# Performance work log

Hardware: AMD Instinct MI355X
Metric: run time of the kernel (lower is better)

The kernel has to match this reference:

```python
import jax, jax.numpy as jnp
import numpy as np

H = 4            # num_attention_heads
EPS_LN = 1e-6    # LayerNorm eps
EPS_IN = 1e-5    # InstanceNorm2d eps (no affine)


def layer_norm(x, g, b):
    m = x.mean(-1, keepdims=True)
    v = ((x - m) ** 2).mean(-1, keepdims=True)
    return (x - m) * jax.lax.rsqrt(v + EPS_LN) * g + b


def instance_norm(s):
    # s: [B,H,C,KV]; InstanceNorm2d(H): normalize per (b,h) over spatial dims (C,KV)
    m = s.mean(axis=(2, 3), keepdims=True)
    v = s.var(axis=(2, 3), keepdims=True)
    return (s - m) * jax.lax.rsqrt(v + EPS_IN)


def _forward(emb1, emb2, emb3, emb4,
             an1_g, an1_b, Wq1, Wo1, fn1_g, fn1_b, fc11_w, fc11_b, fc12_w, fc12_b,
             an2_g, an2_b, Wq2, Wo2, fn2_g, fn2_b, fc21_w, fc21_b, fc22_w, fc22_b,
             an3_g, an3_b, Wq3, Wo3, fn3_g, fn3_b, fc31_w, fc31_b, fc32_w, fc32_b,
             an4_g, an4_b, Wq4, Wo4, fn4_g, fn4_b, fc41_w, fc41_b, fc42_w, fc42_b,
             anA_g, anA_b, Wk, Wv):
    embs = [emb1, emb2, emb3, emb4]
    branches = [
        (an1_g, an1_b, Wq1, Wo1, fn1_g, fn1_b, fc11_w, fc11_b, fc12_w, fc12_b),
        (an2_g, an2_b, Wq2, Wo2, fn2_g, fn2_b, fc21_w, fc21_b, fc22_w, fc22_b),
        (an3_g, an3_b, Wq3, Wo3, fn3_g, fn3_b, fc31_w, fc31_b, fc32_w, fc32_b),
        (an4_g, an4_b, Wq4, Wo4, fn4_g, fn4_b, fc41_w, fc41_b, fc42_w, fc42_b),
    ]
    emb_all = jnp.concatenate(embs, axis=-1)          # [B, n, KV]
    KV = emb_all.shape[-1]
    ea = layer_norm(emb_all, anA_g, anA_b)
    # per-head K/V projections (torch Linear: y = x @ W^T), stacked over heads
    K = jnp.einsum('bnk,hjk->bhnj', ea, Wk)           # [B,H,n,KV]
    V = jnp.einsum('bnk,hjk->bhnj', ea, Wv)           # [B,H,n,KV]
    scale = 1.0 / np.sqrt(KV).astype(np.float32)
    outs = []
    for e, (ag, ab, Wq, Wo, fg, fb, w1, b1, w2, b2) in zip(embs, branches):
        cx = layer_norm(e, ag, ab)                    # [B,n,C]
        Q = jnp.einsum('bnc,hdc->bhnd', cx, Wq)       # [B,H,n,C]
        # channel-attention scores: Q^T K over tokens -> [B,H,C,KV]
        scores = jnp.einsum('bhnd,bhnj->bhdj', Q, K) * scale
        probs = jax.nn.softmax(instance_norm(scores), axis=-1)
        # context [B,H,C,n] averaged over heads -> [B,n,C] (fused into einsum)
        ctx = jnp.einsum('bhdj,bhnj->bnd', probs, V) / H
        O = ctx @ Wo.T                                # out projection
        x = e + O                                     # residual
        h = layer_norm(x, fg, fb)
        h = jax.nn.gelu(h @ w1.T + b1, approximate=False)
        h = h @ w2.T + b2
        outs.append(x + h)                            # FFN residual
    return outs


def setup_inputs() -> dict:
    key = jax.random.key(0)
    B, N = 4, 784
    Cs = [64, 128, 256, 512]
    KV = sum(Cs)
    ks = iter(jax.random.split(key, 64))
    def nrm(shape, scale=0.02):
        return jax.random.normal(next(ks), shape, dtype=jnp.float32) * scale
    inp = {}
    for i, C in enumerate(Cs, 1):
        inp[f'emb{i}'] = jax.random.normal(next(ks), (B, N, C), dtype=jnp.float32)
        inp[f'an{i}_g'] = jnp.ones((C,), jnp.float32)
        inp[f'an{i}_b'] = jnp.zeros((C,), jnp.float32)
        inp[f'Wq{i}'] = nrm((H, C, C))
        inp[f'Wo{i}'] = nrm((C, C))
        inp[f'fn{i}_g'] = jnp.ones((C,), jnp.float32)
        inp[f'fn{i}_b'] = jnp.zeros((C,), jnp.float32)
        inp[f'fc{i}1_w'] = nrm((4 * C, C))
        inp[f'fc{i}1_b'] = nrm((4 * C,), 1e-6)
        inp[f'fc{i}2_w'] = nrm((C, 4 * C))
        inp[f'fc{i}2_b'] = nrm((C,), 1e-6)
    inp['anA_g'] = jnp.ones((KV,), jnp.float32)
    inp['anA_b'] = jnp.zeros((KV,), jnp.float32)
    inp['Wk'] = nrm((H, KV, KV))
    inp['Wv'] = nrm((H, KV, KV))
    return inp


def reference(emb1, emb2, emb3, emb4,
              an1_g, an1_b, Wq1, Wo1, fn1_g, fn1_b, fc11_w, fc11_b, fc12_w, fc12_b,
              an2_g, an2_b, Wq2, Wo2, fn2_g, fn2_b, fc21_w, fc21_b, fc22_w, fc22_b,
              an3_g, an3_b, Wq3, Wo3, fn3_g, fn3_b, fc31_w, fc31_b, fc32_w, fc32_b,
              an4_g, an4_b, Wq4, Wo4, fn4_g, fn4_b, fc41_w, fc41_b, fc42_w, fc42_b,
              anA_g, anA_b, Wk, Wv):
    outs = _forward(emb1, emb2, emb3, emb4,
                    an1_g, an1_b, Wq1, Wo1, fn1_g, fn1_b, fc11_w, fc11_b, fc12_w, fc12_b,
                    an2_g, an2_b, Wq2, Wo2, fn2_g, fn2_b, fc21_w, fc21_b, fc22_w, fc22_b,
                    an3_g, an3_b, Wq3, Wo3, fn3_g, fn3_b, fc31_w, fc31_b, fc32_w, fc32_b,
                    an4_g, an4_b, Wq4, Wo4, fn4_g, fn4_b, fc41_w, fc41_b, fc42_w, fc42_b,
                    anA_g, anA_b, Wk, Wv)
    return tuple(outs)
```

## Files before the change

### kernel.cpp

```cpp
#include <hip/hip_runtime.h>
#include <hip/hip_bf16.h>


using bf16 = __hip_bfloat16;
typedef __attribute__((ext_vector_type(8))) short short8;
typedef __attribute__((ext_vector_type(4))) float f32x4;

__device__ inline float bf2f(unsigned short u) {
    return __uint_as_float(((unsigned int)u) << 16);
}
__device__ inline unsigned short f2b(float f) {
    unsigned int u = __float_as_uint(f);
    return (unsigned short)((u + 0x7fffu + ((u >> 16) & 1u)) >> 16);
}
__device__ inline float ld1f(const float* p) { return *p; }
__device__ inline float ld1f(const bf16* p) { return bf2f(*(const unsigned short*)p); }
__device__ inline void st1(float* p, float v) { *p = v; }
__device__ inline void st1(bf16* p, float v) { *((unsigned short*)p) = f2b(v); }
__device__ inline float4 ld4f(const bf16* p) {
    ushort4 u = *(const ushort4*)p;
    return make_float4(bf2f(u.x), bf2f(u.y), bf2f(u.z), bf2f(u.w));
}

__device__ __forceinline__ void cp16(const void* g, void* l) {
    __builtin_amdgcn_global_load_lds(
        (const __attribute__((address_space(1))) void*)g,
        (__attribute__((address_space(3))) void*)l, 16, 0, 0);
}

__device__ inline float blockSum256(float v, float* red) {
    #pragma unroll
    for (int o = 32; o > 0; o >>= 1) v += __shfl_down(v, o);
    int t = threadIdx.x;
    if ((t & 63) == 0) red[t >> 6] = v;
    __syncthreads();
    float r = red[0] + red[1] + red[2] + red[3];
    __syncthreads();
    return r;
}
__device__ inline float blockMax256(float v, float* red) {
    #pragma unroll
    for (int o = 32; o > 0; o >>= 1) v = fmaxf(v, __shfl_down(v, o));
    int t = threadIdx.x;
    if ((t & 63) == 0) red[t >> 6] = v;
    __syncthreads();
    float r = fmaxf(fmaxf(red[0], red[1]), fmaxf(red[2], red[3]));
    __syncthreads();
    return r;
}

struct CvtN {
    const float* s[18];
    unsigned short* d[18];
    long n[18];
    float* z;
};
__global__ __launch_bounds__(256)
void cvtn_kernel(CvtN a) {
    if (a.z && blockIdx.x == 0 && threadIdx.x < 128) a.z[threadIdx.x] = 0.f;
    long tid = (long)blockIdx.x * 256 + threadIdx.x;
    long stride = (long)gridDim.x * 256;
    for (int g = 0; g < 18; g++) {
        const float* s = a.s[g];
        unsigned short* d = a.d[g];
        long n = a.n[g];
        for (long i = tid * 4; i < n; i += stride * 4) {
            float4 v = *(const float4*)(s + i);
            *(ushort4*)(d + i) = make_ushort4(f2b(v.x), f2b(v.y), f2b(v.z), f2b(v.w));
        }
    }
}

template <class CT, class RT, bool TO>
__global__ __launch_bounds__(256, 3)
void mfma4(const bf16* __restrict__ A, long Ah, long Ab, int lda,
           const bf16* __restrict__ B, long Bh, long Bb, int ldb,
           CT* __restrict__ Cp, long Ch, long Cb, int ldc,
           const float* __restrict__ bias, const RT* __restrict__ res,
           int M, int N, int K, int Mpad, int Npad, int qx, int hy,
           float alpha, int dogelu, float* __restrict__ stat) {
    __shared__ short Asl[3][128][32];
    __shared__ short Bsl[3][128][32];
    int gx = gridDim.x, gy = gridDim.y;
    int orig = ((int)blockIdx.z * gy + (int)blockIdx.y) * gx + (int)blockIdx.x;
    int bx, by, bz;
    if (qx) {
        int c = orig & 7, r2 = orig >> 3;
        bx = (c & 3) * qx + r2 % qx;
        by = (c >> 2) * hy + r2 / qx;
        bz = 0;
    } else {
        int nxy = gx * gy, nwg = nxy * (int)gridDim.z;
        int q = nwg >> 3, r8 = nwg & 7;
        int xcd = orig & 7, pos = orig >> 3;
        int wgid = (xcd < r8 ? xcd * (q + 1) : r8 * (q + 1) + (xcd - r8) * q) + pos;
        bz = wgid / nxy;
        int rem = wgid - bz * nxy;
        by = rem / gx; bx = rem - by * gx;
    }
    int z = bz;
    A += (long)(z & 3) * Ah + (long)(z >> 2) * Ab;
    B += (long)(z & 3) * Bh + (long)(z >> 2) * Bb;
    Cp += (long)(z & 3) * Ch + (long)(z >> 2) * Cb;
    int m0 = by * 128, n0 = bx * 128;
    int t = threadIdx.x, lane = t & 63, wv = t >> 6;
    int col = lane & 15, quad = lane >> 4;
    int wm = wv >> 1, wn = wv & 1;
    f32x4 acc[4][4];
    #pragma unroll
    for (int i = 0; i < 4; i++)
        #pragma unroll
        for (int j = 0; j < 4; j++) acc[i][j] = (f32x4){0.f, 0.f, 0.f, 0.f};

    const bool fA = (m0 + 128 <= Mpad);
    const bool fB = (n0 + 128 <= Npad);
    int srow = lane >> 2;
    int scol = ((lane & 3) ^ ((lane >> 3) & 3)) << 3;
    int rslot = (quad ^ ((col >> 1) & 3)) << 3;

    auto stageA = [&](int s3, int kt) {
        int k0 = kt * 32;
        if (fA && k0 + 32 <= K) {
            #pragma unroll
            for (int r = 0; r < 2; r++) {
                int R0 = (r * 4 + wv) * 16;
                cp16(A + (long)(m0 + R0 + srow) * lda + k0 + scol, &Asl[s3][R0][0]);
            }
        } else {
            #pragma unroll
            for (int r = 0; r < 2; r++) {
                int idx = r * 256 + t;
                int row = idx >> 2, sl = idx & 3;
                int f2 = (row >> 1) & 3;
                short8 v = {};
                if (m0 + row < M && k0 + sl * 8 < K)
                    v = *(const short8*)(A + (long)(m0 + row) * lda + k0 + sl * 8);
                *(short8*)&Asl[s3][row][(sl ^ f2) * 8] = v;
            }
            asm volatile("s_waitcnt lgkmcnt(0)" ::: "memory");
        }
    };
    auto stageB = [&](int s3, int kt) {
        int k0 = kt * 32;
        if (fB && k0 + 32 <= K) {
            #pragma unroll
            for (int r = 0; r < 2; r++) {
                int R0 = (r * 4 + wv) * 16;
                cp16(B + (long)(n0 + R0 + srow) * ldb + k0 + scol, &Bsl[s3][R0][0]);
            }
        } else {
            #pragma unroll
            for (int r = 0; r < 2; r++) {
                int idx = r * 256 + t;
                int row = idx >> 2, sl = idx & 3;
                int f2 = (row >> 1) & 3;
                short8 v = {};
                if (n0 + row < N && k0 + sl * 8 < K)
                    v = *(const short8*)(B + (long)(n0 + row) * ldb + k0 + sl * 8);
                *(short8*)&Bsl[s3][row][(sl ^ f2) * 8] = v;
            }
            asm volatile("s_waitcnt lgkmcnt(0)" ::: "memory");
        }
    };

    int nk = (K + 31) >> 5;
    stageA(0, 0); stageB(0, 0);
    stageA(1, 1); stageB(1, 1);
    __syncthreads();

    for (int kt = 0; kt < nk; kt++) {
        int cur = kt % 3;
        short8 af[4], bf4[4];
        #pragma unroll
        for (int mi = 0; mi < 4; mi++)
            af[mi] = *(const short8*)&Asl[cur][wm * 64 + mi * 16 + col][rslot];
        #pragma unroll
        for (int ni = 0; ni < 4; ni++)
            bf4[ni] = *(const short8*)&Bsl[cur][wn * 64 + ni * 16 + col][rslot];
        int pend = 0;
        if (kt + 2 < nk) {
            int s3 = (kt + 2) % 3;
            stageA(s3, kt + 2); stageB(s3, kt + 2);
            if ((kt + 2) * 32 + 32 <= K) pend = (fA ? 2 : 0) + (fB ? 2 : 0);
        }
        __builtin_amdgcn_s_barrier();
        asm volatile("s_waitcnt lgkmcnt(0)" ::: "memory");
        __builtin_amdgcn_sched_barrier(0);
        __builtin_amdgcn_s_setprio(1);
        #pragma unroll
        for (int mi = 0; mi < 4; mi++)
            #pragma unroll
            for (int ni = 0; ni < 4; ni++)
                acc[mi][ni] = __builtin_amdgcn_mfma_f32_16x16x32_bf16(
                    af[mi], bf4[ni], acc[mi][ni], 0, 0, 0);
        __builtin_amdgcn_s_setprio(0);
        if (kt + 1 < nk) {
            if (pend == 4)      asm volatile("s_waitcnt vmcnt(4)" ::: "memory");
            else if (pend == 2) asm volatile("s_waitcnt vmcnt(2)" ::: "memory");
            else                asm volatile("s_waitcnt vmcnt(0)" ::: "memory");
            __builtin_amdgcn_s_barrier();
        }
    }
    float psum = 0.f, psq = 0.f;
    #pragma unroll
    for (int mi = 0; mi < 4; mi++) {
        int gmB = m0 + wm * 64 + mi * 16 + quad * 4;
        #pragma unroll
        for (int ni = 0; ni < 4; ni++) {
            int gn = n0 + wn * 64 + ni * 16 + col;
            if constexpr (TO) {
                if (gmB < M && gn < N) {
                    ushort4 w = make_ushort4(f2b(acc[mi][ni][0] * alpha),
                                             f2b(acc[mi][ni][1] * alpha),
                                             f2b(acc[mi][ni][2] * alpha),
                                             f2b(acc[mi][ni][3] * alpha));
                    *(ushort4*)((unsigned short*)Cp + (long)gn * ldc + gmB) = w;
                }
            } else {
                if (gn < N) {
                    float bz2 = bias ? bias[gn] : 0.f;
                    #pragma unroll
                    for (int r = 0; r < 4; r++) {
                        int gm = gmB + r;
                        if (gm < M) {
                            float v = acc[mi][ni][r] * alpha + bz2;
                            if (dogelu) v = 0.5f * v * (1.f + erff(v * 0.70710678118f));
                            if (res) v += ld1f(res + (long)gm * ldc + gn);
                            st1(Cp + (long)gm * ldc + gn, v);
                            psum += v; psq += v * v;
                        }
                    }
                }
            }
        }
    }
    if (stat) {
        __syncthreads();
        #pragma unroll
        for (int o = 32; o > 0; o >>= 1) {
            psum += __shfl_down(psum, o);
            psq  += __shfl_down(psq, o);
        }
        float* red = (float*)Asl;
        if ((t & 63) == 0) { red[wv] = psum; red[4 + wv] = psq; }
        __syncthreads();
        if (t == 0) {
            atomicAdd(&stat[2 * z],     red[0] + red[1] + red[2] + red[3]);
            atomicAdd(&stat[2 * z + 1], red[4] + red[5] + red[6] + red[7]);
        }
    }
}

struct G4 {
    const bf16* A[4]; const bf16* B[4]; void* Cv[4];
    const float* bias[4]; const void* res[4];
    int M[4], N[4], K[4], lda[4], ldb[4], ldc[4], nbx[4];
    int cum[5];
};
template <class CT, class RT>
__global__ __launch_bounds__(256, 3)
void mfma4g(G4 gp, int dogelu) {
    __shared__ short Asl[3][128][32];
    __shared__ short Bsl[3][128][32];
    int nwg = gridDim.x;
    int orig = blockIdx.x;
    int q = nwg >> 3, r8 = nwg & 7;
    int xcd = orig & 7, pos = orig >> 3;
    int wgid = (xcd < r8 ? xcd * (q + 1) : r8 * (q + 1) + (xcd - r8) * q) + pos;
    int gi = 0;
    if (wgid >= gp.cum[1]) gi = 1;
    if (wgid >= gp.cum[2]) gi = 2;
    if (wgid >= gp.cum[3]) gi = 3;
    int local = wgid - gp.cum[gi];
    int nbx = gp.nbx[gi];
    int by = local / nbx, bx = local - by * nbx;
    const bf16* A = gp.A[gi];
    const bf16* B = gp.B[gi];
    CT* Cp = (CT*)gp.Cv[gi];
    const float* bias = gp.bias[gi];
    const RT* res = (const RT*)gp.res[gi];
    int M = gp.M[gi], N = gp.N[gi], K = gp.K[gi];
    int lda = gp.lda[gi], ldb = gp.ldb[gi], ldc = gp.ldc[gi];
    int m0 = by * 128, n0 = bx * 128;
    int t = threadIdx.x, lane = t & 63, wv = t >> 6;
    int col = lane & 15, quad = lane >> 4;
    int wm = wv >> 1, wn = wv & 1;
    f32x4 acc[4][4];
    #pragma unroll
    for (int i = 0; i < 4; i++)
        #pragma unroll
        for (int j = 0; j < 4; j++) acc[i][j] = (f32x4){0.f, 0.f, 0.f, 0.f};

    int srow = lane >> 2;
    int scol = ((lane & 3) ^ ((lane >> 3) & 3)) << 3;
    int rslot = (quad ^ ((col >> 1) & 3)) << 3;

    auto stageA = [&](int s3, int kt) {
        int k0 = kt * 32;
        #pragma unroll
        for (int r = 0; r < 2; r++) {
            int R0 = (r * 4 + wv) * 16;
            cp16(A + (long)(m0 + R0 + srow) * lda + k0 + scol, &Asl[s3][R0][0]);
        }
    };
    auto stageB = [&](int s3, int kt) {
        int k0 = kt * 32;
        #pragma unroll
        for (int r = 0; r < 2; r++) {
            int R0 = (r * 4 + wv) * 16;
            cp16(B + (long)(n0 + R0 + srow) * ldb + k0 + scol, &Bsl[s3][R0][0]);
        }
    };

    int nk = K >> 5;
    stageA(0, 0); stageB(0, 0);
    stageA(1, 1); stageB(1, 1);
    __syncthreads();

    for (int kt = 0; kt < nk; kt++) {
        int cur = kt % 3;
        short8 af[4], bf4[4];
        #pragma unroll
        for (int mi = 0; mi < 4; mi++)
            af[mi] = *(const short8*)&Asl[cur][wm * 64 + mi * 16 + col][rslot];
        #pragma unroll
        for (int ni = 0; ni < 4; ni++)
            bf4[ni] = *(const short8*)&Bsl[cur][wn * 64 + ni * 16 + col][rslot];
        bool st = (kt + 2 < nk);
        if (st) {
            int s3 = (kt + 2) % 3;
            stageA(s3, kt + 2); stageB(s3, kt + 2);
        }
        __builtin_amdgcn_s_barrier();
        asm volatile("s_waitcnt lgkmcnt(0)" ::: "memory");
        __builtin_amdgcn_sched_barrier(0);
        __builtin_amdgcn_s_setprio(1);
        #pragma unroll
        for (int mi = 0; mi < 4; mi++)
            #pragma unroll
            for (int ni = 0; ni < 4; ni++)
                acc[mi][ni] = __builtin_amdgcn_mfma_f32_16x16x32_bf16(
                    af[mi], bf4[ni], acc[mi][ni], 0, 0, 0);
        __builtin_amdgcn_s_setprio(0);
        if (kt + 1 < nk) {
            if (st) asm volatile("s_waitcnt vmcnt(4)" ::: "memory");
            else    asm volatile("s_waitcnt vmcnt(0)" ::: "memory");
            __builtin_amdgcn_s_barrier();
        }
    }
    #pragma unroll
    for (int mi = 0; mi < 4; mi++) {
        int gmB = m0 + wm * 64 + mi * 16 + quad * 4;
        #pragma unroll
        for (int ni = 0; ni < 4; ni++) {
            int gn = n0 + wn * 64 + ni * 16 + col;
            if (gn < N) {
                float bz2 = bias ? bias[gn] : 0.f;
                #pragma unroll
                for (int r = 0; r < 4; r++) {
                    int gm = gmB + r;
                    if (gm < M) {
                        float v = acc[mi][ni][r] + bz2;
                        if (dogelu) v = 0.5f * v * (1.f + erff(v * 0.70710678118f));
                        if (res) v += ld1f(res + (long)gm * ldc + gn);
                        st1(Cp + (long)gm * ldc + gn, v);
                    }
                }
            }
        }
    }
}

template <int TM, int TN, class CT, class RT, bool TO>
__global__ __launch_bounds__(256)
void mfma2(const bf16* __restrict__ A, long Ah, long Ab, int lda,
           const bf16* __restrict__ B, long Bh, long Bb, int ldb,
           CT* __restrict__ Cp, long Ch, long Cb, int ldc,
           const float* __restrict__ bias, const RT* __restrict__ res,
           int M, int N, int K, float alpha, int dogelu,
           float* __restrict__ stat) {
    constexpr int MI = TM / 32, NI = TN / 32;
    __shared__ short As[2][TM * 32];
    __shared__ short Bs[2][TN * 32];
    int z = blockIdx.z;
    A += (long)(z & 3) * Ah + (long)(z >> 2) * Ab;
    B += (long)(z & 3) * Bh + (long)(z >> 2) * Bb;
    Cp += (long)(z & 3) * Ch + (long)(z >> 2) * Cb;
    int m0 = blockIdx.y * TM, n0 = blockIdx.x * TN;
    int t = threadIdx.x, lane = t & 63, wv = t >> 6;
    int col = lane & 15, quad = lane >> 4;
    int wm = wv >> 1, wn = wv & 1;
    f32x4 acc[MI][NI];
    #pragma unroll
    for (int i = 0; i < MI; i++)
        #pragma unroll
        for (int j = 0; j < NI; j++) acc[i][j] = (f32x4){0.f, 0.f, 0.f, 0.f};

    const bool fastblk = (m0 + TM <= M) && (n0 + TN <= N);
    int lrow = lane >> 2;
    int lcol = ((lane & 3) ^ ((lane >> 3) & 3)) << 3;
    int sr = t >> 2;
    int swz = ((t & 3) ^ ((t >> 3) & 3)) << 3;
    int sdst = (t & 3) << 3;
    int rdslot = (quad ^ ((col >> 1) & 3)) << 3;

    auto stage = [&](int b, int k0) {
        if (fastblk && (k0 + 32 <= K)) {
            #pragma unroll
            for (int u = 0; u < TM / 64; u++) {
                int c = wv + 4 * u;
                int r = c * 16 + lrow;
                cp16(A + (long)(m0 + r) * lda + k0 + lcol, &As[b][c * 512]);
            }
            #pragma unroll
            for (int u = 0; u < TN / 64; u++) {
                int c = wv + 4 * u;
                int r = c * 16 + lrow;
                cp16(B + (long)(n0 + r) * ldb + k0 + lcol, &Bs[b][c * 512]);
            }
        } else {
            #pragma unroll
            for (int u = 0; u < TM / 64; u++) {
                int r = sr + u * 64;
                float4 v = make_float4(0.f, 0.f, 0.f, 0.f);
                if (m0 + r < M && k0 + swz < K)
                    v = *(const float4*)(A + (long)(m0 + r) * lda + k0 + swz);
                *(float4*)&As[b][r * 32 + sdst] = v;
            }
            #pragma unroll
            for (int u = 0; u < TN / 64; u++) {
                int r = sr + u * 64;
                float4 v = make_float4(0.f, 0.f, 0.f, 0.f);
                if (n0 + r < N && k0 + swz < K)
                    v = *(const float4*)(B + (long)(n0 + r) * ldb + k0 + swz);
                *(float4*)&Bs[b][r * 32 + sdst] = v;
            }
        }
    };

    int nk = (K + 31) >> 5;
    stage(0, 0);
    __syncthreads();
    int cur = 0;
    for (int s = 0; s < nk; s++) {
        if (s + 1 < nk) stage(cur ^ 1, (s + 1) * 32);
        short8 af[MI], bfr[NI];
        #pragma unroll
        for (int mi = 0; mi < MI; mi++)
            af[mi] = *(const short8*)&As[cur][(wm * (TM / 2) + mi * 16 + col) * 32 + rdslot];
        #pragma unroll
        for (int ni = 0; ni < NI; ni++)
            bfr[ni] = *(const short8*)&Bs[cur][(wn * (TN / 2) + ni * 16 + col) * 32 + rdslot];
        #pragma unroll
        for (int mi = 0; mi < MI; mi++)
            #pragma unroll
            for (int ni = 0; ni < NI; ni++)
                acc[mi][ni] = __builtin_amdgcn_mfma_f32_16x16x32_bf16(
                    af[mi], bfr[ni], acc[mi][ni], 0, 0, 0);
        if (s + 1 < nk) __syncthreads();
        cur ^= 1;
    }
    float psum = 0.f, psq = 0.f;
    #pragma unroll
    for (int mi = 0; mi < MI; mi++) {
        int gmB = m0 + wm * (TM / 2) + mi * 16 + quad * 4;
        #pragma unroll
        for (int ni = 0; ni < NI; ni++) {
            int gn = n0 + wn * (TN / 2) + ni * 16 + col;
            if constexpr (TO) {
                if (gmB < M && gn < N) {
                    ushort4 w = make_ushort4(f2b(acc[mi][ni][0] * alpha),
                                             f2b(acc[mi][ni][1] * alpha),
                                             f2b(acc[mi][ni][2] * alpha),
                                             f2b(acc[mi][ni][3] * alpha));
                    *(ushort4*)((unsigned short*)Cp + (long)gn * ldc + gmB) = w;
                }
            } else {
                if (gn < N) {
                    float bz = bias ? bias[gn] : 0.f;
                    #pragma unroll
                    for (int r = 0; r < 4; r++) {
                        int gm = gmB + r;
                        if (gm < M) {
                            float v = acc[mi][ni][r] * alpha + bz;
                            if (dogelu) v = 0.5f * v * (1.f + erff(v * 0.70710678118f));
                            if (res) v += ld1f(res + (long)gm * ldc + gn);
                            st1(Cp + (long)gm * ldc + gn, v);
                            psum += v; psq += v * v;
                        }
                    }
                }
            }
        }
    }
    if (stat) {
        __syncthreads();
        #pragma unroll
        for (int o = 32; o > 0; o >>= 1) {
            psum += __shfl_down(psum, o);
            psq  += __shfl_down(psq, o);
        }
        float* red = (float*)As;
        if ((t & 63) == 0) { red[wv] = psum; red[4 + wv] = psq; }
        __syncthreads();
        if (t == 0) {
            atomicAdd(&stat[2 * z],     red[0] + red[1] + red[2] + red[3]);
            atomicAdd(&stat[2 * z + 1], red[4] + red[5] + red[6] + red[7]);
        }
    }
}

struct LNA {
    const float* e[4];
    const float* ag[4];
    const float* ab[4];
    const float* cg;
    const float* cbb;
    bf16* y[4];
    bf16* ea;
};
__global__ __launch_bounds__(256)
void ln_all_kernel(LNA a) {
    __shared__ float x[960];
    __shared__ float red[4];
    long row = blockIdx.x;
    int t = threadIdx.x;
    const int off[5] = {0, 64, 192, 448, 960};
    {
        const float* p1 = a.e[0] + row * 64;
        const float* p2 = a.e[1] + row * 128;
        const float* p3 = a.e[2] + row * 256;
        const float* p4 = a.e[3] + row * 512;
        if (t < 64) x[t] = p1[t];
        for (int i = t; i < 128; i += 256) x[64 + i]  = p2[i];
        for (int i = t; i < 256; i += 256) x[192 + i] = p3[i];
        for (int i = t; i < 512; i += 256) x[448 + i] = p4[i];
    }
    __syncthreads();
    float ssum[4], ssq[4];
    #pragma unroll
    for (int br = 0; br < 4; br++) {
        float s = 0.f, q = 0.f;
        for (int i = off[br] + t; i < off[br + 1]; i += 256) {
            float v = x[i]; s += v; q += v * v;
        }
        ssum[br] = blockSum256(s, red);
        ssq[br]  = blockSum256(q, red);
    }
    float S1 = ssum[0] + ssum[1] + ssum[2] + ssum[3];
    float S2 = ssq[0] + ssq[1] + ssq[2] + ssq[3];
    float muA = S1 * (1.f / 960.f);
    float rA = rsqrtf(S2 * (1.f / 960.f) - muA * muA + 1e-6f);
    for (int i = t; i < 960; i += 256)
        st1(a.ea + row * 960 + i, (x[i] - muA) * rA * a.cg[i] + a.cbb[i]);
    #pragma unroll
    for (int br = 0; br < 4; br++) {
        int C = off[br + 1] - off[br];
        float mu = ssum[br] / C;
        float rr = rsqrtf(ssq[br] / C - mu * mu + 1e-6f);
        const float* g = a.ag[br];
        const float* b = a.ab[br];
        bf16* y = a.y[br] + row * C;
        for (int i = t; i < C; i += 256)
            st1(y + i, (x[off[br] + i] - mu) * rr * g[i] + b[i]);
    }
}

struct LR4 {
    const bf16* X[4];
    const float* g[4];
    const float* b[4];
    bf16* Y[4];
    int C[4];
};
__global__ __launch_bounds__(256)
void ln_rows4_kernel(LR4 a) {
    __shared__ float x[512];
    __shared__ float red[4];
    int br = blockIdx.y;
    long row = blockIdx.x;
    int C = a.C[br];
    int t = threadIdx.x;
    const bf16* xr = a.X[br] + row * C;
    float s = 0.f, q = 0.f;
    for (int i = t; i < C; i += 256) { float v = ld1f(xr + i); x[i] = v; s += v; q += v * v; }
    float S1 = blockSum256(s, red), S2 = blockSum256(q, red);
    float mu = S1 / C;
    float r = rsqrtf(S2 / C - mu * mu + 1e-6f);
    const float* g = a.g[br];
    const float* b = a.b[br];
    bf16* y = a.Y[br] + row * C;
    for (int i = t; i < C; i += 256)
        st1(y + i, (x[i] - mu) * r * g[i] + b[i]);
}

__global__ __launch_bounds__(256)
void ctx_sum_kernel(const bf16* __restrict__ tmp, bf16* __restrict__ ctx, long NTC) {
    long i = ((long)blockIdx.x * 256 + threadIdx.x) * 4;
    float4 a = ld4f(tmp + i);
    float4 b = ld4f(tmp + NTC + i);
    float4 c = ld4f(tmp + 2 * NTC + i);
    float4 d = ld4f(tmp + 3 * NTC + i);
    ushort4 o = make_ushort4(f2b((a.x + b.x + c.x + d.x) * 0.25f),
                             f2b((a.y + b.y + c.y + d.y) * 0.25f),
                             f2b((a.z + b.z + c.z + d.z) * 0.25f),
                             f2b((a.w + b.w + c.w + d.w) * 0.25f));
    *(ushort4*)(ctx + i) = o;
}

__global__ __launch_bounds__(256)
void softmax_kernel(bf16* __restrict__ S, const float* __restrict__ stat, int C) {
    __shared__ float x[960];
    __shared__ float red[4];
    long r = blockIdx.x;
    int t = threadIdx.x;
    int z = (int)(r / C);
    int d = (int)(r % C);
    float n = 960.f * (float)C;
    float s0 = stat[2 * z], q0 = stat[2 * z + 1];
    float mu = s0 / n;
    float rs = rsqrtf(q0 / n - mu * mu + 1e-5f);
    int h = z & 3, b = z >> 2;
    bf16* row = S + (long)b * C * 3840 + (long)d * 3840 + h * 960;
    float mx = -3.4e38f;
    for (int i = t; i < 960; i += 256) {
        float v = ld1f(row + i) * rs; x[i] = v; mx = fmaxf(mx, v);
    }
    float M = blockMax256(mx, red);
    float s = 0.f;
    for (int i = t; i < 960; i += 256) { float e = __expf(x[i] - M); x[i] = e; s += e; }
    float Ssum = blockSum256(s, red);
    float inv = 1.f / Ssum;
    for (int i = t; i < 960; i += 256) st1(row + i, x[i] * inv);
}

extern "C" void kernel_launch(void* const* d_in, const int* in_sizes, int n_in,
                              void* d_out, int out_size, void* d_ws, size_t ws_size,
                              hipStream_t stream) {
    (void)in_sizes; (void)n_in; (void)out_size; (void)ws_size;
    const int Cs[4] = {64, 128, 256, 512};
    const float *emb[4], *ang[4], *anb[4], *Wq[4], *Wo[4], *fng[4], *fnb[4], *w1[4], *b1[4], *w2[4], *b2[4];
    for (int i = 0; i < 4; i++) {
        const int base = i * 11;
        emb[i] = (const float*)d_in[base + 0];
        ang[i] = (const float*)d_in[base + 1];
        anb[i] = (const float*)d_in[base + 2];
        Wq[i]  = (const float*)d_in[base + 3];
        Wo[i]  = (const float*)d_in[base + 4];
        fng[i] = (const float*)d_in[base + 5];
        fnb[i] = (const float*)d_in[base + 6];
        w1[i]  = (const float*)d_in[base + 7];
        b1[i]  = (const float*)d_in[base + 8];
        w2[i]  = (const float*)d_in[base + 9];
        b2[i]  = (const float*)d_in[base + 10];
    }
    const float* anAg = (const float*)d_in[44];
    const float* anAb = (const float*)d_in[45];
    const float* Wk   = (const float*)d_in[46];
    const float* Wv   = (const float*)d_in[47];

    const int NT = 3136;
    char* wsb = (char*)d_ws;
    unsigned short* wp = (unsigned short*)(wsb);
    float* statb = (float*)(wsb + 9052160);
    bf16*  KT    = (bf16*)(wsb + 9053184);
    bf16*  hid   = (bf16*)(wsb + 9053184);
    bf16*  Vb2   = (bf16*)(wsb + 33137664);
    bf16*  xball = (bf16*)(wsb + 33137664);
    bf16*  cx3   = (bf16*)(wsb + 39158784);
    bf16*  QT    = (bf16*)(wsb + 57222144);
    bf16*  wkb   = (bf16*)(wsb + 57222144);
    bf16*  Sb    = (bf16*)(wsb + 70067200);
    bf16*  ea    = (bf16*)(wsb + 70067200);
    bf16*  wvb   = (bf16*)(wsb + 76088320);
    bf16*  cxall = (bf16*)(wsb + 85795840);
    bf16*  cx2   = (bf16*)(wsb + 91816960);

    const long wb[4] = {0, 53248, 266240, 1118208};
    const long co[4] = {0, 64L * NT, 192L * NT, 448L * NT};
    const long ho[4] = {0, 802816, 2408448, 5619712};

    float* out = (float*)d_out;
    const long ooff[4] = {0, 200704, 602112, 1404928};
    const float scale = 0.03227486121f;

    {
        CvtN a;
        a.s[0] = Wk; a.d[0] = (unsigned short*)wkb; a.n[0] = 3686400;
        a.s[1] = Wv; a.d[1] = (unsigned short*)wvb; a.n[1] = 3686400;
        for (int i = 0; i < 4; i++) {
            const long C2 = (long)Cs[i] * Cs[i];
            a.s[2 + 4 * i] = Wq[i]; a.d[2 + 4 * i] = wp + wb[i];          a.n[2 + 4 * i] = 4 * C2;
            a.s[3 + 4 * i] = Wo[i]; a.d[3 + 4 * i] = wp + wb[i] + 4 * C2; a.n[3 + 4 * i] = C2;
            a.s[4 + 4 * i] = w1[i]; a.d[4 + 4 * i] = wp + wb[i] + 5 * C2; a.n[4 + 4 * i] = 4 * C2;
            a.s[5 + 4 * i] = w2[i]; a.d[5 + 4 * i] = wp + wb[i] + 9 * C2; a.n[5 + 4 * i] = 4 * C2;
        }
        a.z = statb;
        cvtn_kernel<<<1024, 256, 0, stream>>>(a);
    }
    {
        LNA a;
        for (int i = 0; i < 4; i++) {
            a.e[i] = emb[i]; a.ag[i] = ang[i]; a.ab[i] = anb[i];
            a.y[i] = cxall + co[i];
        }
        a.cg = anAg; a.cbb = anAb; a.ea = ea;
        ln_all_kernel<<<3136, 256, 0, stream>>>(a);
    }
    mfma4<bf16, float, true><<<dim3(32, 26, 1), 256, 0, stream>>>(
        ea, 0, 0, 960, wkb, 0, 0, 960, KT, 0, 0, NT,
        nullptr, (const float*)nullptr, NT, 3840, 960, 3328, 4096, 8, 13,
        1.f, 0, nullptr);
    mfma4<bf16, float, false><<<dim3(32, 26, 1), 256, 0, stream>>>(
        ea, 0, 0, 960, wvb, 0, 0, 960, Vb2, 0, 0, 3840,
        nullptr, (const float*)nullptr, NT, 3840, 960, 3328, 4096, 8, 13,
        1.f, 0, nullptr);

    for (int i = 0; i < 4; i++) {
        const int C = Cs[i];
        const long C2 = (long)C * C;
        bf16* wqb = (bf16*)(wp + wb[i]);
        float* st = statb + 32 * i;
        if (C >= 128) {
            mfma4<bf16, float, true><<<dim3(C / 128, 26, 4), 256, 0, stream>>>(
                cxall + co[i], 0, 0, C, wqb, C2, 0, C, QT, (long)C * NT, 0, NT,
                nullptr, (const float*)nullptr, NT, C, C, 3328, C, 0, 0,
                1.f, 0, nullptr);
            mfma4<bf16, float, false><<<dim3(8, C / 128, 16), 256, 0, stream>>>(
                QT, (long)C * NT, 784, NT, KT, 3010560, 784, NT,
                Sb, 960, (long)C * 3840, 3840,
                nullptr, (const float*)nullptr, C, 960, 784, C, 1024, 0, 0,
                scale, 0, st);
        } else {
            mfma2<64, 64, bf16, float, true><<<dim3(1, 49, 4), 256, 0, stream>>>(
                cxall + co[i], 0, 0, C, wqb, C2, 0, C, QT, (long)C * NT, 0, NT,
                nullptr, (const float*)nullptr, NT, C, C, 1.f, 0, nullptr);
            mfma2<64, 64, bf16, float, false><<<dim3(15, 1, 16), 256, 0, stream>>>(
                QT, (long)C * NT, 784, NT, KT, 3010560, 784, NT,
                Sb, 960, (long)C * 3840, 3840,
                nullptr, (const float*)nullptr, C, 960, 784, scale, 0, st);
        }
        softmax_kernel<<<16 * C, 256, 0, stream>>>(Sb, st, C);
        if (C >= 128)
            mfma4<bf16, float, false><<<dim3(C / 128, 7, 16), 256, 0, stream>>>(
                Vb2, 960, 784L * 3840, 3840, Sb, 960, (long)C * 3840, 3840,
                QT, (long)NT * C, 784L * C, C,
                nullptr, (const float*)nullptr, 784, C, 960, 896, C, 0, 0,
                1.f, 0, nullptr);
        else
            mfma2<64, 64, bf16, float, false><<<dim3(1, 13, 16), 256, 0, stream>>>(
                Vb2, 960, 784L * 3840, 3840, Sb, 960, (long)C * 3840, 3840,
                QT, (long)NT * C, 784L * C, C,
                nullptr, (const float*)nullptr, 784, C, 960, 1.f, 0, nullptr);
        ctx_sum_kernel<<<(int)(((long)NT * C) / 1024), 256, 0, stream>>>(
            QT, cx2 + co[i], (long)NT * C);
    }

    {
        G4 g;
        int cum = 0;
        for (int i = 0; i < 4; i++) {
            const int C = Cs[i];
            const long C2 = (long)C * C;
            g.A[i] = cx2 + co[i]; g.B[i] = (const bf16*)(wp + wb[i] + 4 * C2);
            g.Cv[i] = xball + co[i];
            g.bias[i] = nullptr; g.res[i] = emb[i];
            g.M[i] = NT; g.N[i] = C; g.K[i] = C;
            g.lda[i] = C; g.ldb[i] = C; g.ldc[i] = C;
            g.nbx[i] = (C >= 128) ? C / 128 : 1;
            g.cum[i] = cum; cum += g.nbx[i] * 26;
        }
        g.cum[4] = cum;
        mfma4g<bf16, float><<<cum, 256, 0, stream>>>(g, 0);
    }
    {
        LR4 a;
        for (int i = 0; i < 4; i++) {
            a.X[i] = xball + co[i]; a.g[i] = fng[i]; a.b[i] = fnb[i];
            a.Y[i] = cx3 + co[i]; a.C[i] = Cs[i];
        }
        ln_rows4_kernel<<<dim3(3136, 4), 256, 0, stream>>>(a);
    }
    {
        G4 g;
        int cum = 0;
        for (int i = 0; i < 4; i++) {
            const int C = Cs[i];
            const long C2 = (long)C * C;
            g.A[i] = cx3 + co[i]; g.B[i] = (const bf16*)(wp + wb[i] + 5 * C2);
            g.Cv[i] = hid + ho[i];
            g.bias[i] = b1[i]; g.res[i] = nullptr;
            g.M[i] = NT; g.N[i] = 4 * C; g.K[i] = C;
            g.lda[i] = C; g.ldb[i] = C; g.ldc[i] = 4 * C;
            g.nbx[i] = 4 * C / 128;
            g.cum[i] = cum; cum += g.nbx[i] * 26;
        }
        g.cum[4] = cum;
        mfma4g<bf16, float><<<cum, 256, 0, stream>>>(g, 1);
    }
    {
        G4 g;
        int cum = 0;
        for (int i = 0; i < 4; i++) {
            const int C = Cs[i];
            const long C2 = (long)C * C;
            g.A[i] = hid + ho[i]; g.B[i] = (const bf16*)(wp + wb[i] + 9 * C2);
            g.Cv[i] = out + ooff[i];
            g.bias[i] = b2[i]; g.res[i] = xball + co[i];
            g.M[i] = NT; g.N[i] = C; g.K[i] = 4 * C;
            g.lda[i] = 4 * C; g.ldb[i] = 4 * C; g.ldc[i] = C;
            g.nbx[i] = (C >= 128) ? C / 128 : 1;
            g.cum[i] = cum; cum += g.nbx[i] * 26;
        }
        g.cum[4] = cum;
        mfma4g<float, bf16><<<cum, 256, 0, stream>>>(g, 0);
    }
}
```

Measured before the change: 740.5 us.

## Fuse K and V projections into one 256x256-tile MFMA GEMM kernel

Replaces the two separate 128-tile GEMM launches for the K and V projections with a single 512-thread kernel. It uses 256x256 tiles and a double-buffered LDS pipeline that splits each 64-wide k-step into halves, with priority hints around the MFMA bursts. Wk and Wv are laid out contiguously so the combined N=7680 weight matrix can be treated as one GEMM. The epilogue routes columns below 3840 to the transposed K buffer and the rest to V. The goal is more data reuse per tile and one fewer launch, at the cost of higher register and LDS pressure and uncoalesced scalar V stores.

```diff
diff --git a/kernel.cpp b/kernel.cpp
--- a/kernel.cpp
+++ b/kernel.cpp
@@ -67,6 +67,154 @@
         for (long i = tid * 4; i < n; i += stride * 4) {
             float4 v = *(const float4*)(s + i);
             *(ushort4*)(d + i) = make_ushort4(f2b(v.x), f2b(v.y), f2b(v.z), f2b(v.w));
+        }
+    }
+}
+
+__global__ __launch_bounds__(512, 2)
+void mfma8kv(const bf16* __restrict__ A, const bf16* __restrict__ B,
+             bf16* __restrict__ KT, bf16* __restrict__ V) {
+    __shared__ short Asl[2][2][256][32];
+    __shared__ short Bsl[2][2][256][32];
+    const int M = 3136, N = 7680, lda = 960, ldb = 960;
+    int orig = (int)blockIdx.y * 32 + (int)blockIdx.x;
+    int c = orig & 7, r2 = orig >> 3;
+    int bx = (c & 3) * 8 + (r2 & 7);
+    int by = (c >> 2) * 7 + (r2 >> 3);
+    int m0 = by * 256, n0 = bx * 256;
+    if (m0 >= M || n0 >= N) return;
+    int t = threadIdx.x, lane = t & 63, wv = t >> 6;
+    int col = lane & 15, quad = lane >> 4;
+    int wm = wv >> 2, wn = wv & 3;
+    f32x4 acc[8][4];
+    #pragma unroll
+    for (int i = 0; i < 8; i++)
+        #pragma unroll
+        for (int j = 0; j < 4; j++) acc[i][j] = (f32x4){0.f, 0.f, 0.f, 0.f};
+
+    int srow = lane >> 2;
+    int scol = ((lane & 3) ^ ((lane >> 3) & 3)) << 3;
+    int rslot = (quad ^ ((col >> 1) & 3)) << 3;
+
+    auto stageA = [&](int s2, int kt, int kh) {
+        int k0 = kt * 64 + kh * 32;
+        #pragma unroll
+        for (int r = 0; r < 2; r++) {
+            int R0 = (r * 8 + wv) * 16;
+            cp16(A + (long)(m0 + R0 + srow) * lda + k0 + scol, &Asl[s2][kh][R0][0]);
+        }
+    };
+    auto stageB = [&](int s2, int kt, int kh) {
+        int k0 = kt * 64 + kh * 32;
+        #pragma unroll
+        for (int r = 0; r < 2; r++) {
+            int R0 = (r * 8 + wv) * 16;
+            cp16(B + (long)(n0 + R0 + srow) * ldb + k0 + scol, &Bsl[s2][kh][R0][0]);
+        }
+    };
+
+    const int nk = 15;
+    stageA(0, 0, 0); stageB(0, 0, 0); stageA(0, 0, 1); stageB(0, 0, 1);
+    __syncthreads();
+
+    for (int kt = 0; kt < nk; kt++) {
+        int cur = kt & 1, nxt = cur ^ 1;
+        bool st = (kt + 1 < nk);
+        short8 af[8], bf8[4];
+        #pragma unroll
+        for (int ni = 0; ni < 4; ni++)
+            bf8[ni] = *(const short8*)&Bsl[cur][0][wn * 64 + ni * 16 + col][rslot];
+        #pragma unroll
+        for (int mi = 0; mi < 4; mi++)
+            af[mi] = *(const short8*)&Asl[cur][0][wm * 128 + mi * 16 + col][rslot];
+        if (st) stageA(nxt, kt + 1, 0);
+        __builtin_amdgcn_s_barrier();
+        asm volatile("s_waitcnt lgkmcnt(0)" ::: "memory");
+        __builtin_amdgcn_sched_barrier(0);
+        __builtin_amdgcn_s_setprio(1);
+        #pragma unroll
+        for (int mi = 0; mi < 4; mi++)
+            #pragma unroll
+            for (int ni = 0; ni < 4; ni++)
+                acc[mi][ni] = __builtin_amdgcn_mfma_f32_16x16x32_bf16(
+                    af[mi], bf8[ni], acc[mi][ni], 0, 0, 0);
+        __builtin_amdgcn_s_setprio(0);
+        __builtin_amdgcn_s_barrier();
+        #pragma unroll
+        for (int mi = 4; mi < 8; mi++)
+            af[mi] = *(const short8*)&Asl[cur][0][wm * 128 + mi * 16 + col][rslot];
+        if (st) stageB(nxt, kt + 1, 0);
+        __builtin_amdgcn_s_barrier();
+        asm volatile("s_waitcnt lgkmcnt(0)" ::: "memory");
+        __builtin_amdgcn_sched_barrier(0);
+        __builtin_amdgcn_s_setprio(1);
+        #pragma unroll
+        for (int mi = 4; mi < 8; mi++)
+            #pragma unroll
+            for (int ni = 0; ni < 4; ni++)
+                acc[mi][ni] = __builtin_amdgcn_mfma_f32_16x16x32_bf16(
+                    af[mi], bf8[ni], acc[mi][ni], 0, 0, 0);
+        __builtin_amdgcn_s_setprio(0);
+        if (st) asm volatile("s_waitcnt vmcnt(4)" ::: "memory");
+        else    asm volatile("s_waitcnt vmcnt(0)" ::: "memory");
+        __builtin_amdgcn_s_barrier();
+        #pragma unroll
+        for (int ni = 0; ni < 4; ni++)
+            bf8[ni] = *(const short8*)&Bsl[cur][1][wn * 64 + ni * 16 + col][rslot];
+        #pragma unroll
+        for (int mi = 0; mi < 4; mi++)
+            af[mi] = *(const short8*)&Asl[cur][1][wm * 128 + mi * 16 + col][rslot];
+        if (st) stageA(nxt, kt + 1, 1);
+        __builtin_amdgcn_s_barrier();
+        asm volatile("s_waitcnt lgkmcnt(0)" ::: "memory");
+        __builtin_amdgcn_sched_barrier(0);
+        __builtin_amdgcn_s_setprio(1);
+        #pragma unroll
+        for (int mi = 0; mi < 4; mi++)
+            #pragma unroll
+            for (int ni = 0; ni < 4; ni++)
+                acc[mi][ni] = __builtin_amdgcn_mfma_f32_16x16x32_bf16(
+                    af[mi], bf8[ni], acc[mi][ni], 0, 0, 0);
+        __builtin_amdgcn_s_setprio(0);
+        __builtin_amdgcn_s_barrier();
+        #pragma unroll
+        for (int mi = 4; mi < 8; mi++)
+            af[mi] = *(const short8*)&Asl[cur][1][wm * 128 + mi * 16 + col][rslot];
+        if (st) stageB(nxt, kt + 1, 1);
+        __builtin_amdgcn_s_barrier();
+        asm volatile("s_waitcnt lgkmcnt(0)" ::: "memory");
+        __builtin_amdgcn_sched_barrier(0);
+        __builtin_amdgcn_s_setprio(1);
+        #pragma unroll
+        for (int mi = 4; mi < 8; mi++)
+            #pragma unroll
+            for (int ni = 0; ni < 4; ni++)
+                acc[mi][ni] = __builtin_amdgcn_mfma_f32_16x16x32_bf16(
+                    af[mi], bf8[ni], acc[mi][ni], 0, 0, 0);
+        __builtin_amdgcn_s_setprio(0);
+        if (st) asm volatile("s_waitcnt vmcnt(4)" ::: "memory");
+        __builtin_amdgcn_s_barrier();
+    }
+    #pragma unroll
+    for (int mi = 0; mi < 8; mi++) {
+        int gmB = m0 + wm * 128 + mi * 16 + quad * 4;
+        #pragma unroll
+        for (int ni = 0; ni < 4; ni++) {
+            int gn = n0 + wn * 64 + ni * 16 + col;
+            if (gn < 3840) {
+                if (gmB < M) {
+                    ushort4 w = make_ushort4(f2b(acc[mi][ni][0]), f2b(acc[mi][ni][1]),
+                                             f2b(acc[mi][ni][2]), f2b(acc[mi][ni][3]));
+                    *(ushort4*)((unsigned short*)KT + (long)gn * M + gmB) = w;
+                }
+            } else {
+                int vn = gn - 3840;
+                #pragma unroll
+                for (int r = 0; r < 4; r++) {
+                    int gm = gmB + r;
+                    if (gm < M) st1(V + (long)gm * 3840 + vn, acc[mi][ni][r]);
+                }
+            }
         }
     }
 }
@@ -669,10 +817,9 @@
     bf16*  xball = (bf16*)(wsb + 33137664);
     bf16*  cx3   = (bf16*)(wsb + 39158784);
     bf16*  QT    = (bf16*)(wsb + 57222144);
-    bf16*  wkb   = (bf16*)(wsb + 57222144);
+    bf16*  wkv   = (bf16*)(wsb + 57222144);
     bf16*  Sb    = (bf16*)(wsb + 70067200);
-    bf16*  ea    = (bf16*)(wsb + 70067200);
-    bf16*  wvb   = (bf16*)(wsb + 76088320);
+    bf16*  ea    = (bf16*)(wsb + 71967744);
     bf16*  cxall = (bf16*)(wsb + 85795840);
     bf16*  cx2   = (bf16*)(wsb + 91816960);
 
@@ -686,8 +833,8 @@
 
     {
         CvtN a;
-        a.s[0] = Wk; a.d[0] = (unsigned short*)wkb; a.n[0] = 3686400;
-        a.s[1] = Wv; a.d[1] = (unsigned short*)wvb; a.n[1] = 3686400;
+        a.s[0] = Wk; a.d[0] = (unsigned short*)wkv;           a.n[0] = 3686400;
+        a.s[1] = Wv; a.d[1] = (unsigned short*)wkv + 3686400; a.n[1] = 3686400;
         for (int i = 0; i < 4; i++) {
             const long C2 = (long)Cs[i] * Cs[i];
             a.s[2 + 4 * i] = Wq[i]; a.d[2 + 4 * i] = wp + wb[i];          a.n[2 + 4 * i] = 4 * C2;
@@ -707,14 +854,7 @@
         a.cg = anAg; a.cbb = anAb; a.ea = ea;
         ln_all_kernel<<<3136, 256, 0, stream>>>(a);
     }
-    mfma4<bf16, float, true><<<dim3(32, 26, 1), 256, 0, stream>>>(
-        ea, 0, 0, 960, wkb, 0, 0, 960, KT, 0, 0, NT,
-        nullptr, (const float*)nullptr, NT, 3840, 960, 3328, 4096, 8, 13,
-        1.f, 0, nullptr);
-    mfma4<bf16, float, false><<<dim3(32, 26, 1), 256, 0, stream>>>(
-        ea, 0, 0, 960, wvb, 0, 0, 960, Vb2, 0, 0, 3840,
-        nullptr, (const float*)nullptr, NT, 3840, 960, 3328, 4096, 8, 13,
-        1.f, 0, nullptr);
+    mfma8kv<<<dim3(32, 14, 1), 512, 0, stream>>>(ea, wkv, KT, Vb2);
 
     for (int i = 0; i < 4; i++) {
         const int C = Cs[i];
```

Result: faster. 721.5 us (-2.6%).
